# Kernel optimization log

Measured on AMD Instinct MI355X. Metric: run time of the kernel, lower is better.

The kernel has to match this reference:

```python
import jax, jax.numpy as jnp
import numpy as np
import math

D = 1024
B, S = 8, 2048


def setup_inputs() -> dict:
    key = jax.random.key(0)
    ks = jax.random.split(key, 8)
    q = jax.random.normal(ks[0], (B, S, D), dtype=jnp.float32)
    k = jax.random.normal(ks[1], (B, S, D), dtype=jnp.float32)
    v1 = jax.random.normal(ks[2], (B, S, D), dtype=jnp.float32)
    mask = jax.random.normal(ks[3], (1, S, S), dtype=jnp.float32)
    # Linear params: torch Linear stores W as [out, in]; init ~ U(-1/sqrt(in), 1/sqrt(in))
    lim = 1.0 / math.sqrt(D)
    W1 = jax.random.uniform(ks[4], (D, D), jnp.float32, -lim, lim)
    b1 = jax.random.uniform(ks[5], (D,), jnp.float32, -lim, lim)
    W2 = jax.random.uniform(ks[6], (D, D), jnp.float32, -lim, lim)
    b2 = jax.random.uniform(ks[7], (D,), jnp.float32, -lim, lim)
    return {"q": q, "k": k, "v1": v1, "mask": mask,
            "W1": W1, "b1": b1, "W2": W2, "b2": b2}


def _proj(x, W1, b1, W2, b2):
    # linear2(linear1(x)); torch Linear: x @ W.T + b
    h = jnp.einsum('bsd,od->bso', x, W1) + b1
    return jnp.einsum('bsd,od->bso', h, W2) + b2


def reference(q, k, v1, mask, W1, b1, W2, b2):
    qp = _proj(q, W1, b1, W2, b2)          # [B,S,D]
    kp = _proj(k, W1, b1, W2, b2)          # [B,S,D]
    scale = 1.0 / math.sqrt(qp.shape[-1])
    qk = jnp.einsum('bqd,bkd->bqk', qp, kp) * scale  # [B,S,S]
    qk = qk + mask                          # broadcast [1,S,S]
    attn = jax.nn.softmax(qk, axis=-1)
    return jnp.einsum('bqk,bkd->bqd', attn, v1)  # [B,S,D]
```

## Files before the change

kernel.cpp:

```cpp
#include <hip/hip_runtime.h>
#include <hip/hip_bf16.h>

typedef __hip_bfloat16 bf16;
typedef __bf16 bf16x8 __attribute__((ext_vector_type(8)));
typedef float f32x4 __attribute__((ext_vector_type(4)));

constexpr int Bn = 8, Sn = 2048, Dn = 1024;
constexpr int BM = 128, BN = 128, BK = 64;

__global__ void cast_f32_bf16_k(const float* __restrict__ x, bf16* __restrict__ y, int n) {
  int i = (blockIdx.x * blockDim.x + threadIdx.x) * 4;
  if (i >= n) return;
  float4 f = *reinterpret_cast<const float4*>(x + i);
  bf16 tmp[4] = {__float2bfloat16(f.x), __float2bfloat16(f.y),
                 __float2bfloat16(f.z), __float2bfloat16(f.w)};
  *reinterpret_cast<short4*>(y + i) = *reinterpret_cast<const short4*>(tmp);
}

__global__ void transpose_cast_v_k(const float* __restrict__ v, bf16* __restrict__ vt) {
  __shared__ float tile[32][33];
  const int s0 = blockIdx.x * 32, d0 = blockIdx.y * 32, b = blockIdx.z;
  const float* src = v + (size_t)b * Sn * Dn;
  bf16* dst = vt + (size_t)b * Dn * Sn;
  const int tx = threadIdx.x & 31, ty = threadIdx.x >> 5;
  #pragma unroll
  for (int i = 0; i < 4; ++i) {
    int s = ty + i * 8;
    tile[s][tx] = src[(size_t)(s0 + s) * Dn + d0 + tx];
  }
  __syncthreads();
  #pragma unroll
  for (int i = 0; i < 4; ++i) {
    int d = ty + i * 8;
    dst[(size_t)(d0 + d) * Sn + s0 + tx] = __float2bfloat16(tile[tx][d]);
  }
}

#define SBAR()  asm volatile("s_barrier" ::: "memory")
#define LGKM0() asm volatile("s_waitcnt lgkmcnt(0)" ::: "memory")
#define VM0()   asm volatile("s_waitcnt vmcnt(0)" ::: "memory")

#define MFMA16() do {                                                         \
    __builtin_amdgcn_s_setprio(1);                                            \
    _Pragma("unroll")                                                         \
    for (int kk = 0; kk < 2; ++kk)                                            \
      _Pragma("unroll")                                                       \
      for (int mi4 = 0; mi4 < 4; ++mi4)                                       \
        _Pragma("unroll")                                                     \
        for (int n2 = 0; n2 < 2; ++n2)                                        \
          acc[mi4][n2] = __builtin_amdgcn_mfma_f32_16x16x32_bf16(             \
              aF[mi4][kk], bF[n2][kk], acc[mi4][n2], 0, 0, 0);                \
    __builtin_amdgcn_s_setprio(0);                                            \
  } while (0)

#define ITER(cur, T) do {                                                     \
    const bool pf = (T) + 1 < NT;                                             \
    if (pf) {                                                                 \
      stage2((1 - (cur)) * 32768,         Abase, (T) + 1);                    \
      stage2((1 - (cur)) * 32768 + 16384, Bbase, (T) + 1);                    \
    }                                                                         \
    _Pragma("unroll")                                                         \
    for (int mi4 = 0; mi4 < 4; ++mi4) {                                       \
      aF[mi4][0] = *reinterpret_cast<const bf16x8*>(pA0 + (cur)*32768 + mi4*2048); \
      aF[mi4][1] = *reinterpret_cast<const bf16x8*>(pA1 + (cur)*32768 + mi4*2048); \
    }                                                                         \
    _Pragma("unroll")                                                         \
    for (int j = 0; j < 2; ++j) {                                             \
      bF[j][0] = *reinterpret_cast<const bf16x8*>(pB0 + (cur)*32768 + j*2048); \
      bF[j][1] = *reinterpret_cast<const bf16x8*>(pB1 + (cur)*32768 + j*2048); \
    }                                                                         \
    LGKM0();                                                                  \
    MFMA16();                                                                 \
    if (pf) VM0();                                                            \
    SBAR();                                                                   \
  } while (0)

template<int EPI>
__global__ __launch_bounds__(512, 4)
void gemm128_k(const bf16* __restrict__ A, const bf16* __restrict__ BT,
               void* __restrict__ Cv, const float* __restrict__ aux,
               int N, int K, long long sAz, long long sBz, long long sCz,
               float scale, int gx, int gy)
{
  __shared__ __align__(128) bf16 sh[2 * 16384];

  const int nwg = (int)gridDim.x;
  const int flat = (int)blockIdx.x;
  const int swz = (flat & 7) * (nwg >> 3) + (flat >> 3);
  const int tn = swz % gx;
  const int rem = swz / gx;
  const int tm = rem % gy;
  const int z  = rem / gy;

  const int t = threadIdx.x, w = t >> 6, lane = t & 63;
  const int wm = w >> 2, wn = w & 3;
  const int fr = lane & 15, kg = lane >> 4;
  const int m0 = tm * BM, n0 = tn * BN;
  const bf16* Abase = A + (size_t)z * sAz + (size_t)m0 * K;
  const bf16* Bbase = BT + (size_t)z * sBz + (size_t)n0 * K;

  f32x4 acc[4][2];
  const f32x4 fz = {0.f, 0.f, 0.f, 0.f};
  #pragma unroll
  for (int i = 0; i < 4; ++i) { acc[i][0] = fz; acc[i][1] = fz; }
  bf16x8 aF[4][2], bF[2][2];

  const char* shB = (const char*)sh;
  const int swzlo = (fr & 3) << 4;
  const int swzhi = (fr & 4) << 4;
  const int aoff0 = (wm * 64 + fr) * 128 + ((kg * 16) ^ swzlo) + swzhi;
  const int boff0 = 16384 + (wn * 32 + fr) * 128 + ((kg * 16) ^ swzlo) + swzhi;
  const char* pA0 = shB + aoff0;
  const char* pA1 = shB + (aoff0 ^ 64);
  const char* pB0 = shB + boff0;
  const char* pB1 = shB + (boff0 ^ 64);

  int gOff[2];
  #pragma unroll
  for (int i = 0; i < 2; ++i) {
    const int slot = i * 512 + w * 64 + lane;
    const int row = slot >> 3;
    const int cb = (slot & 7) ^ (row & 7);
    gOff[i] = row * K + cb * 8;
  }
  auto stage2 = [&](int dstByte, const bf16* gbase, int kt) {
    const bf16* g0 = gbase + (size_t)kt * BK;
    char* db = (char*)sh + dstByte;
    #pragma unroll
    for (int i = 0; i < 2; ++i) {
      __builtin_amdgcn_global_load_lds(
          (__attribute__((address_space(1))) void*)(g0 + gOff[i]),
          (__attribute__((address_space(3))) void*)(db + (i * 512 + w * 64) * 16),
          16, 0, 0);
    }
  };

  const int NT = K / BK;
  stage2(0,     Abase, 0);
  stage2(16384, Bbase, 0);
  VM0();
  SBAR();

  for (int T = 0; T < NT; T += 2) {
    ITER(0, T);
    ITER(1, T + 1);
  }

  const int or0 = kg * 4;
  if constexpr (EPI == 0) {
    bf16* C = (bf16*)Cv + (size_t)z * sCz;
    #pragma unroll
    for (int mi = 0; mi < 4; ++mi)
      #pragma unroll
      for (int r = 0; r < 4; ++r) {
        const int row = m0 + wm * 64 + mi * 16 + or0 + r;
        #pragma unroll
        for (int nj = 0; nj < 2; ++nj) {
          const int col = n0 + wn * 32 + nj * 16 + fr;
          C[(size_t)row * N + col] = __float2bfloat16(acc[mi][nj][r] + aux[col]);
        }
      }
  } else if constexpr (EPI == 1) {
    bf16* C = (bf16*)Cv + (size_t)z * sCz;
    #pragma unroll
    for (int mi = 0; mi < 4; ++mi)
      #pragma unroll
      for (int r = 0; r < 4; ++r) {
        const int row = m0 + wm * 64 + mi * 16 + or0 + r;
        #pragma unroll
        for (int nj = 0; nj < 2; ++nj) {
          const int col = n0 + wn * 32 + nj * 16 + fr;
          float v = acc[mi][nj][r] * scale + aux[(size_t)row * N + col];
          C[(size_t)row * N + col] = __float2bfloat16(v);
        }
      }
  } else {
    float* C = (float*)Cv + (size_t)z * sCz;
    #pragma unroll
    for (int mi = 0; mi < 4; ++mi)
      #pragma unroll
      for (int r = 0; r < 4; ++r) {
        const int row = m0 + wm * 64 + mi * 16 + or0 + r;
        #pragma unroll
        for (int nj = 0; nj < 2; ++nj) {
          const int col = n0 + wn * 32 + nj * 16 + fr;
          C[(size_t)row * N + col] = acc[mi][nj][r];
        }
      }
  }
}

__global__ __launch_bounds__(256)
void softmax_rows_k(bf16* __restrict__ sc) {
  const size_t row = blockIdx.x;
  bf16* p = sc + row * (size_t)Sn;
  const int t = threadIdx.x;
  unsigned short raw[8];
  *reinterpret_cast<int4*>(raw) = *reinterpret_cast<const int4*>(p + t * 8);
  float x[8];
  float m = -1e30f;
  #pragma unroll
  for (int j = 0; j < 8; ++j) {
    x[j] = __uint_as_float(((unsigned)raw[j]) << 16);
    m = fmaxf(m, x[j]);
  }
  #pragma unroll
  for (int off = 32; off >= 1; off >>= 1) m = fmaxf(m, __shfl_xor(m, off));
  __shared__ float sred[4], ssum[4];
  const int w = t >> 6;
  if ((t & 63) == 0) sred[w] = m;
  __syncthreads();
  m = fmaxf(fmaxf(sred[0], sred[1]), fmaxf(sred[2], sred[3]));
  float e[8], s = 0.f;
  #pragma unroll
  for (int j = 0; j < 8; ++j) { e[j] = __expf(x[j] - m); s += e[j]; }
  #pragma unroll
  for (int off = 32; off >= 1; off >>= 1) s += __shfl_xor(s, off);
  if ((t & 63) == 0) ssum[w] = s;
  __syncthreads();
  s = (ssum[0] + ssum[1]) + (ssum[2] + ssum[3]);
  const float inv = 1.f / s;
  unsigned short o[8];
  #pragma unroll
  for (int j = 0; j < 8; ++j) {
    bf16 hv = __float2bfloat16(e[j] * inv);
    o[j] = *reinterpret_cast<unsigned short*>(&hv);
  }
  *reinterpret_cast<int4*>(p + t * 8) = *reinterpret_cast<const int4*>(o);
}

extern "C" void kernel_launch(void* const* d_in, const int* in_sizes, int n_in,
                              void* d_out, int out_size, void* d_ws, size_t ws_size,
                              hipStream_t stream) {
  const float* q    = (const float*)d_in[0];
  const float* k    = (const float*)d_in[1];
  const float* v1   = (const float*)d_in[2];
  const float* mask = (const float*)d_in[3];
  const float* W1   = (const float*)d_in[4];
  const float* b1   = (const float*)d_in[5];
  const float* W2   = (const float*)d_in[6];
  const float* b2   = (const float*)d_in[7];
  float* out = (float*)d_out;

  const size_t nQKD = (size_t)Bn * Sn * Dn;
  char* ws = (char*)d_ws;
  bf16* qkb = (bf16*)ws;
  bf16* qb  = qkb;
  bf16* kb  = qkb + nQKD;
  bf16* vtb = qkb + 2 * nQKD;
  bf16* hb  = vtb + nQKD;
  bf16* w1b = hb + 2 * nQKD;
  bf16* w2b = w1b + (size_t)Dn * Dn;
  bf16* scb = w2b + (size_t)Dn * Dn;

  dim3 blk(256);
  const int nQK = (int)nQKD;
  cast_f32_bf16_k<<<dim3(nQK / 4 / 256), blk, 0, stream>>>(q, qb, nQK);
  cast_f32_bf16_k<<<dim3(nQK / 4 / 256), blk, 0, stream>>>(k, kb, nQK);
  cast_f32_bf16_k<<<dim3(Dn * Dn / 4 / 256), blk, 0, stream>>>(W1, w1b, Dn * Dn);
  cast_f32_bf16_k<<<dim3(Dn * Dn / 4 / 256), blk, 0, stream>>>(W2, w2b, Dn * Dn);
  transpose_cast_v_k<<<dim3(Sn / 32, Dn / 32, Bn), blk, 0, stream>>>(v1, vtb);

  const int M2 = 2 * Bn * Sn;
  dim3 gblk(512);
  gemm128_k<0><<<dim3((Dn / BN) * (M2 / BM)), gblk, 0, stream>>>(
      qkb, w1b, hb, b1, Dn, Dn, 0, 0, 0, 1.f, Dn / BN, M2 / BM);
  gemm128_k<0><<<dim3((Dn / BN) * (M2 / BM)), gblk, 0, stream>>>(
      hb, w2b, qkb, b2, Dn, Dn, 0, 0, 0, 1.f, Dn / BN, M2 / BM);
  gemm128_k<1><<<dim3(16 * 16 * Bn), gblk, 0, stream>>>(
      qb, kb, scb, mask, Sn, Dn,
      (long long)Sn * Dn, (long long)Sn * Dn, (long long)Sn * Sn, 0.03125f, 16, 16);
  softmax_rows_k<<<dim3(Bn * Sn), blk, 0, stream>>>(scb);
  gemm128_k<2><<<dim3(8 * 16 * Bn), gblk, 0, stream>>>(
      scb, vtb, out, nullptr, Dn, Sn,
      (long long)Sn * Sn, (long long)Dn * Sn, (long long)Sn * Dn, 1.f, 8, 16);
}
```

Before: 402.4 us.

## Fuse softmax into GEMM epilogues and switch to triple-buffered BK=32 pipeline

Result: slower. 427.6 us (+6.3%).

```diff
diff --git a/kernel.cpp b/kernel.cpp
--- a/kernel.cpp
+++ b/kernel.cpp
@@ -6,7 +6,6 @@
 typedef float f32x4 __attribute__((ext_vector_type(4)));
 
 constexpr int Bn = 8, Sn = 2048, Dn = 1024;
-constexpr int BM = 128, BN = 128, BK = 64;
 
 __global__ void cast_f32_bf16_k(const float* __restrict__ x, bf16* __restrict__ y, int n) {
   int i = (blockIdx.x * blockDim.x + threadIdx.x) * 4;
@@ -38,51 +37,17 @@
 
 #define SBAR()  asm volatile("s_barrier" ::: "memory")
 #define LGKM0() asm volatile("s_waitcnt lgkmcnt(0)" ::: "memory")
+#define VM2()   asm volatile("s_waitcnt vmcnt(2)" ::: "memory")
 #define VM0()   asm volatile("s_waitcnt vmcnt(0)" ::: "memory")
 
-#define MFMA16() do {                                                         \
-    __builtin_amdgcn_s_setprio(1);                                            \
-    _Pragma("unroll")                                                         \
-    for (int kk = 0; kk < 2; ++kk)                                            \
-      _Pragma("unroll")                                                       \
-      for (int mi4 = 0; mi4 < 4; ++mi4)                                       \
-        _Pragma("unroll")                                                     \
-        for (int n2 = 0; n2 < 2; ++n2)                                        \
-          acc[mi4][n2] = __builtin_amdgcn_mfma_f32_16x16x32_bf16(             \
-              aF[mi4][kk], bF[n2][kk], acc[mi4][n2], 0, 0, 0);                \
-    __builtin_amdgcn_s_setprio(0);                                            \
-  } while (0)
-
-#define ITER(cur, T) do {                                                     \
-    const bool pf = (T) + 1 < NT;                                             \
-    if (pf) {                                                                 \
-      stage2((1 - (cur)) * 32768,         Abase, (T) + 1);                    \
-      stage2((1 - (cur)) * 32768 + 16384, Bbase, (T) + 1);                    \
-    }                                                                         \
-    _Pragma("unroll")                                                         \
-    for (int mi4 = 0; mi4 < 4; ++mi4) {                                       \
-      aF[mi4][0] = *reinterpret_cast<const bf16x8*>(pA0 + (cur)*32768 + mi4*2048); \
-      aF[mi4][1] = *reinterpret_cast<const bf16x8*>(pA1 + (cur)*32768 + mi4*2048); \
-    }                                                                         \
-    _Pragma("unroll")                                                         \
-    for (int j = 0; j < 2; ++j) {                                             \
-      bF[j][0] = *reinterpret_cast<const bf16x8*>(pB0 + (cur)*32768 + j*2048); \
-      bF[j][1] = *reinterpret_cast<const bf16x8*>(pB1 + (cur)*32768 + j*2048); \
-    }                                                                         \
-    LGKM0();                                                                  \
-    MFMA16();                                                                 \
-    if (pf) VM0();                                                            \
-    SBAR();                                                                   \
-  } while (0)
-
-template<int EPI>
-__global__ __launch_bounds__(512, 4)
+template<int EPI, int K>
+__global__ __launch_bounds__(512, 6)
 void gemm128_k(const bf16* __restrict__ A, const bf16* __restrict__ BT,
                void* __restrict__ Cv, const float* __restrict__ aux,
-               int N, int K, long long sAz, long long sBz, long long sCz,
+               int N, long long sAz, long long sBz, long long sCz,
                float scale, int gx, int gy)
 {
-  __shared__ __align__(128) bf16 sh[2 * 16384];
+  __shared__ __align__(128) bf16 sh[3 * 8192];
 
   const int nwg = (int)gridDim.x;
   const int flat = (int)blockIdx.x;
@@ -95,7 +60,7 @@
   const int t = threadIdx.x, w = t >> 6, lane = t & 63;
   const int wm = w >> 2, wn = w & 3;
   const int fr = lane & 15, kg = lane >> 4;
-  const int m0 = tm * BM, n0 = tn * BN;
+  const int m0 = tm * 128, n0 = tn * 128;
   const bf16* Abase = A + (size_t)z * sAz + (size_t)m0 * K;
   const bf16* Bbase = BT + (size_t)z * sBz + (size_t)n0 * K;
 
@@ -103,47 +68,53 @@
   const f32x4 fz = {0.f, 0.f, 0.f, 0.f};
   #pragma unroll
   for (int i = 0; i < 4; ++i) { acc[i][0] = fz; acc[i][1] = fz; }
-  bf16x8 aF[4][2], bF[2][2];
+  bf16x8 aF[4], bF[2];
 
   const char* shB = (const char*)sh;
-  const int swzlo = (fr & 3) << 4;
-  const int swzhi = (fr & 4) << 4;
-  const int aoff0 = (wm * 64 + fr) * 128 + ((kg * 16) ^ swzlo) + swzhi;
-  const int boff0 = 16384 + (wn * 32 + fr) * 128 + ((kg * 16) ^ swzlo) + swzhi;
-  const char* pA0 = shB + aoff0;
-  const char* pA1 = shB + (aoff0 ^ 64);
-  const char* pB0 = shB + boff0;
-  const char* pB1 = shB + (boff0 ^ 64);
-
-  int gOff[2];
-  #pragma unroll
-  for (int i = 0; i < 2; ++i) {
-    const int slot = i * 512 + w * 64 + lane;
-    const int row = slot >> 3;
-    const int cb = (slot & 7) ^ (row & 7);
-    gOff[i] = row * K + cb * 8;
-  }
-  auto stage2 = [&](int dstByte, const bf16* gbase, int kt) {
-    const bf16* g0 = gbase + (size_t)kt * BK;
-    char* db = (char*)sh + dstByte;
-    #pragma unroll
-    for (int i = 0; i < 2; ++i) {
-      __builtin_amdgcn_global_load_lds(
-          (__attribute__((address_space(1))) void*)(g0 + gOff[i]),
-          (__attribute__((address_space(3))) void*)(db + (i * 512 + w * 64) * 16),
-          16, 0, 0);
+  const char* pA = shB + (wm * 64 + fr) * 64 + kg * 16;
+  const char* pB = shB + 8192 + (wn * 32 + fr) * 64 + kg * 16;
+
+  const int gOff = (t >> 2) * K + (t & 3) * 8;
+  const int dOff = t * 16;
+  auto stage = [&](int dstByte, const bf16* gbase, int kt) {
+    const bf16* g0 = gbase + kt * 32;
+    __builtin_amdgcn_global_load_lds(
+        (__attribute__((address_space(1))) void*)(g0 + gOff),
+        (__attribute__((address_space(3))) void*)((char*)sh + dstByte + dOff),
+        16, 0, 0);
+  };
+
+  constexpr int NT = K / 32;
+  stage(0,     Abase, 0); stage(8192,         Bbase, 0);
+  stage(16384, Abase, 1); stage(16384 + 8192, Bbase, 1);
+  VM2();
+  SBAR();
+
+  #pragma unroll
+  for (int T = 0; T < NT; ++T) {
+    const int bb = (T % 3) * 16384;
+    if (T + 2 < NT) {
+      const int pb = ((T + 2) % 3) * 16384;
+      stage(pb,        Abase, T + 2);
+      stage(pb + 8192, Bbase, T + 2);
     }
-  };
-
-  const int NT = K / BK;
-  stage2(0,     Abase, 0);
-  stage2(16384, Bbase, 0);
-  VM0();
-  SBAR();
-
-  for (int T = 0; T < NT; T += 2) {
-    ITER(0, T);
-    ITER(1, T + 1);
+    #pragma unroll
+    for (int mi4 = 0; mi4 < 4; ++mi4)
+      aF[mi4] = *reinterpret_cast<const bf16x8*>(pA + bb + mi4 * 1024);
+    #pragma unroll
+    for (int nj = 0; nj < 2; ++nj)
+      bF[nj] = *reinterpret_cast<const bf16x8*>(pB + bb + nj * 1024);
+    LGKM0();
+    __builtin_amdgcn_s_setprio(1);
+    #pragma unroll
+    for (int mi4 = 0; mi4 < 4; ++mi4)
+      #pragma unroll
+      for (int nj = 0; nj < 2; ++nj)
+        acc[mi4][nj] = __builtin_amdgcn_mfma_f32_16x16x32_bf16(
+            aF[mi4], bF[nj], acc[mi4][nj], 0, 0, 0);
+    __builtin_amdgcn_s_setprio(0);
+    if (T + 2 < NT) { VM2(); } else if (T + 1 < NT) { VM0(); }
+    SBAR();
   }
 
   const int or0 = kg * 4;
@@ -170,63 +141,44 @@
         #pragma unroll
         for (int nj = 0; nj < 2; ++nj) {
           const int col = n0 + wn * 32 + nj * 16 + fr;
-          float v = acc[mi][nj][r] * scale + aux[(size_t)row * N + col];
+          float v = __expf(acc[mi][nj][r] * scale + aux[(size_t)row * N + col]);
           C[(size_t)row * N + col] = __float2bfloat16(v);
         }
       }
   } else {
     float* C = (float*)Cv + (size_t)z * sCz;
+    const float* Zb = aux + (size_t)z * Sn;
     #pragma unroll
     for (int mi = 0; mi < 4; ++mi)
       #pragma unroll
       for (int r = 0; r < 4; ++r) {
         const int row = m0 + wm * 64 + mi * 16 + or0 + r;
+        const float invZ = 1.0f / Zb[row];
         #pragma unroll
         for (int nj = 0; nj < 2; ++nj) {
           const int col = n0 + wn * 32 + nj * 16 + fr;
-          C[(size_t)row * N + col] = acc[mi][nj][r];
+          C[(size_t)row * N + col] = acc[mi][nj][r] * invZ;
         }
       }
   }
 }
 
 __global__ __launch_bounds__(256)
-void softmax_rows_k(bf16* __restrict__ sc) {
+void rowsum_k(const bf16* __restrict__ sc, float* __restrict__ Z) {
   const size_t row = blockIdx.x;
-  bf16* p = sc + row * (size_t)Sn;
+  const bf16* p = sc + row * (size_t)Sn;
   const int t = threadIdx.x;
   unsigned short raw[8];
   *reinterpret_cast<int4*>(raw) = *reinterpret_cast<const int4*>(p + t * 8);
-  float x[8];
-  float m = -1e30f;
-  #pragma unroll
-  for (int j = 0; j < 8; ++j) {
-    x[j] = __uint_as_float(((unsigned)raw[j]) << 16);
-    m = fmaxf(m, x[j]);
-  }
-  #pragma unroll
-  for (int off = 32; off >= 1; off >>= 1) m = fmaxf(m, __shfl_xor(m, off));
-  __shared__ float sred[4], ssum[4];
-  const int w = t >> 6;
-  if ((t & 63) == 0) sred[w] = m;
+  float s = 0.f;
+  #pragma unroll
+  for (int j = 0; j < 8; ++j) s += __uint_as_float(((unsigned)raw[j]) << 16);
+  #pragma unroll
+  for (int off = 32; off >= 1; off >>= 1) s += __shfl_xor(s, off);
+  __shared__ float ssum[4];
+  if ((t & 63) == 0) ssum[t >> 6] = s;
   __syncthreads();
-  m = fmaxf(fmaxf(sred[0], sred[1]), fmaxf(sred[2], sred[3]));
-  float e[8], s = 0.f;
-  #pragma unroll
-  for (int j = 0; j < 8; ++j) { e[j] = __expf(x[j] - m); s += e[j]; }
-  #pragma unroll
-  for (int off = 32; off >= 1; off >>= 1) s += __shfl_xor(s, off);
-  if ((t & 63) == 0) ssum[w] = s;
-  __syncthreads();
-  s = (ssum[0] + ssum[1]) + (ssum[2] + ssum[3]);
-  const float inv = 1.f / s;
-  unsigned short o[8];
-  #pragma unroll
-  for (int j = 0; j < 8; ++j) {
-    bf16 hv = __float2bfloat16(e[j] * inv);
-    o[j] = *reinterpret_cast<unsigned short*>(&hv);
-  }
-  *reinterpret_cast<int4*>(p + t * 8) = *reinterpret_cast<const int4*>(o);
+  if (t == 0) Z[row] = (ssum[0] + ssum[1]) + (ssum[2] + ssum[3]);
 }
 
 extern "C" void kernel_launch(void* const* d_in, const int* in_sizes, int n_in,
@@ -252,6 +204,7 @@
   bf16* w1b = hb + 2 * nQKD;
   bf16* w2b = w1b + (size_t)Dn * Dn;
   bf16* scb = w2b + (size_t)Dn * Dn;
+  float* Zb = (float*)(scb + (size_t)Bn * Sn * Sn);
 
   dim3 blk(256);
   const int nQK = (int)nQKD;
@@ -263,15 +216,15 @@
 
   const int M2 = 2 * Bn * Sn;
   dim3 gblk(512);
-  gemm128_k<0><<<dim3((Dn / BN) * (M2 / BM)), gblk, 0, stream>>>(
-      qkb, w1b, hb, b1, Dn, Dn, 0, 0, 0, 1.f, Dn / BN, M2 / BM);
-  gemm128_k<0><<<dim3((Dn / BN) * (M2 / BM)), gblk, 0, stream>>>(
-      hb, w2b, qkb, b2, Dn, Dn, 0, 0, 0, 1.f, Dn / BN, M2 / BM);
-  gemm128_k<1><<<dim3(16 * 16 * Bn), gblk, 0, stream>>>(
-      qb, kb, scb, mask, Sn, Dn,
+  gemm128_k<0, Dn><<<dim3((Dn / 128) * (M2 / 128)), gblk, 0, stream>>>(
+      qkb, w1b, hb, b1, Dn, 0, 0, 0, 1.f, Dn / 128, M2 / 128);
+  gemm128_k<0, Dn><<<dim3((Dn / 128) * (M2 / 128)), gblk, 0, stream>>>(
+      hb, w2b, qkb, b2, Dn, 0, 0, 0, 1.f, Dn / 128, M2 / 128);
+  gemm128_k<1, Dn><<<dim3(16 * 16 * Bn), gblk, 0, stream>>>(
+      qb, kb, scb, mask, Sn,
       (long long)Sn * Dn, (long long)Sn * Dn, (long long)Sn * Sn, 0.03125f, 16, 16);
-  softmax_rows_k<<<dim3(Bn * Sn), blk, 0, stream>>>(scb);
-  gemm128_k<2><<<dim3(8 * 16 * Bn), gblk, 0, stream>>>(
-      scb, vtb, out, nullptr, Dn, Sn,
+  rowsum_k<<<dim3(Bn * Sn), blk, 0, stream>>>(scb, Zb);
+  gemm128_k<2, Sn><<<dim3(8 * 16 * Bn), gblk, 0, stream>>>(
+      scb, vtb, out, Zb, Dn,
       (long long)Sn * Sn, (long long)Dn * Sn, (long long)Sn * Dn, 1.f, 8, 16);
 }
```

## Compose the two linear layers into one weight and defer softmax normalization

Applied to the files above, without the earlier changes.

New measurement: 341.3 us. -15.2%, faster.

```diff
diff --git a/kernel.cpp b/kernel.cpp
--- a/kernel.cpp
+++ b/kernel.cpp
@@ -7,6 +7,16 @@
 
 constexpr int Bn = 8, Sn = 2048, Dn = 1024;
 constexpr int BM = 128, BN = 128, BK = 64;
+
+__global__ void cast2_f32_bf16_k(const float* __restrict__ x0, const float* __restrict__ x1,
+                                 bf16* __restrict__ y, int n ) {
+  int i = (blockIdx.x * blockDim.x + threadIdx.x) * 4;
+  const float* src = (i < n) ? (x0 + i) : (x1 + (i - n));
+  float4 f = *reinterpret_cast<const float4*>(src);
+  bf16 tmp[4] = {__float2bfloat16(f.x), __float2bfloat16(f.y),
+                 __float2bfloat16(f.z), __float2bfloat16(f.w)};
+  *reinterpret_cast<short4*>(y + i) = *reinterpret_cast<const short4*>(tmp);
+}
 
 __global__ void cast_f32_bf16_k(const float* __restrict__ x, bf16* __restrict__ y, int n) {
   int i = (blockIdx.x * blockDim.x + threadIdx.x) * 4;
@@ -17,23 +27,40 @@
   *reinterpret_cast<short4*>(y + i) = *reinterpret_cast<const short4*>(tmp);
 }
 
-__global__ void transpose_cast_v_k(const float* __restrict__ v, bf16* __restrict__ vt) {
+__global__ void transpose_cast_k(const float* __restrict__ src0, bf16* __restrict__ dst0,
+                                 int R, int C) {
   __shared__ float tile[32][33];
-  const int s0 = blockIdx.x * 32, d0 = blockIdx.y * 32, b = blockIdx.z;
-  const float* src = v + (size_t)b * Sn * Dn;
-  bf16* dst = vt + (size_t)b * Dn * Sn;
+  const int r0 = blockIdx.x * 32, c0 = blockIdx.y * 32, b = blockIdx.z;
+  const float* src = src0 + (size_t)b * R * C;
+  bf16* dst = dst0 + (size_t)b * C * R;
   const int tx = threadIdx.x & 31, ty = threadIdx.x >> 5;
   #pragma unroll
   for (int i = 0; i < 4; ++i) {
-    int s = ty + i * 8;
-    tile[s][tx] = src[(size_t)(s0 + s) * Dn + d0 + tx];
+    int r = ty + i * 8;
+    tile[r][tx] = src[(size_t)(r0 + r) * C + c0 + tx];
   }
   __syncthreads();
   #pragma unroll
   for (int i = 0; i < 4; ++i) {
-    int d = ty + i * 8;
-    dst[(size_t)(d0 + d) * Sn + s0 + tx] = __float2bfloat16(tile[tx][d]);
-  }
+    int c = ty + i * 8;
+    dst[(size_t)(c0 + c) * R + r0 + tx] = __float2bfloat16(tile[tx][c]);
+  }
+}
+
+__global__ __launch_bounds__(256)
+void bias_compose_k(const float* __restrict__ W2, const float* __restrict__ b1,
+                    const float* __restrict__ b2, float* __restrict__ bc) {
+  const int row = blockIdx.x;
+  const int t = threadIdx.x;
+  float4 wv = *reinterpret_cast<const float4*>(W2 + (size_t)row * Dn + t * 4);
+  float4 bv = *reinterpret_cast<const float4*>(b1 + t * 4);
+  float s = wv.x * bv.x + wv.y * bv.y + wv.z * bv.z + wv.w * bv.w;
+  #pragma unroll
+  for (int off = 32; off >= 1; off >>= 1) s += __shfl_xor(s, off);
+  __shared__ float ssum[4];
+  if ((t & 63) == 0) ssum[t >> 6] = s;
+  __syncthreads();
+  if (t == 0) bc[row] = (ssum[0] + ssum[1]) + (ssum[2] + ssum[3]) + b2[row];
 }
 
 #define SBAR()  asm volatile("s_barrier" ::: "memory")
@@ -170,63 +197,57 @@
         #pragma unroll
         for (int nj = 0; nj < 2; ++nj) {
           const int col = n0 + wn * 32 + nj * 16 + fr;
-          float v = acc[mi][nj][r] * scale + aux[(size_t)row * N + col];
+          float v = __expf(acc[mi][nj][r] * scale + aux[(size_t)row * N + col]);
           C[(size_t)row * N + col] = __float2bfloat16(v);
         }
       }
+  } else if constexpr (EPI == 2) {
+    float* C = (float*)Cv + (size_t)z * sCz;
+    const float* Zb = aux + (size_t)z * Sn;
+    #pragma unroll
+    for (int mi = 0; mi < 4; ++mi)
+      #pragma unroll
+      for (int r = 0; r < 4; ++r) {
+        const int row = m0 + wm * 64 + mi * 16 + or0 + r;
+        const float invZ = 1.0f / Zb[row];
+        #pragma unroll
+        for (int nj = 0; nj < 2; ++nj) {
+          const int col = n0 + wn * 32 + nj * 16 + fr;
+          C[(size_t)row * N + col] = acc[mi][nj][r] * invZ;
+        }
+      }
   } else {
-    float* C = (float*)Cv + (size_t)z * sCz;
-    #pragma unroll
-    for (int mi = 0; mi < 4; ++mi)
-      #pragma unroll
-      for (int r = 0; r < 4; ++r) {
-        const int row = m0 + wm * 64 + mi * 16 + or0 + r;
-        #pragma unroll
-        for (int nj = 0; nj < 2; ++nj) {
-          const int col = n0 + wn * 32 + nj * 16 + fr;
-          C[(size_t)row * N + col] = acc[mi][nj][r];
+    bf16* C = (bf16*)Cv + (size_t)z * sCz;
+    #pragma unroll
+    for (int mi = 0; mi < 4; ++mi)
+      #pragma unroll
+      for (int r = 0; r < 4; ++r) {
+        const int row = m0 + wm * 64 + mi * 16 + or0 + r;
+        #pragma unroll
+        for (int nj = 0; nj < 2; ++nj) {
+          const int col = n0 + wn * 32 + nj * 16 + fr;
+          C[(size_t)row * N + col] = __float2bfloat16(acc[mi][nj][r]);
         }
       }
   }
 }
 
 __global__ __launch_bounds__(256)
-void softmax_rows_k(bf16* __restrict__ sc) {
+void rowsum_k(const bf16* __restrict__ sc, float* __restrict__ Z) {
   const size_t row = blockIdx.x;
-  bf16* p = sc + row * (size_t)Sn;
+  const bf16* p = sc + row * (size_t)Sn;
   const int t = threadIdx.x;
   unsigned short raw[8];
   *reinterpret_cast<int4*>(raw) = *reinterpret_cast<const int4*>(p + t * 8);
-  float x[8];
-  float m = -1e30f;
-  #pragma unroll
-  for (int j = 0; j < 8; ++j) {
-    x[j] = __uint_as_float(((unsigned)raw[j]) << 16);
-    m = fmaxf(m, x[j]);
-  }
-  #pragma unroll
-  for (int off = 32; off >= 1; off >>= 1) m = fmaxf(m, __shfl_xor(m, off));
-  __shared__ float sred[4], ssum[4];
-  const int w = t >> 6;
-  if ((t & 63) == 0) sred[w] = m;
+  float s = 0.f;
+  #pragma unroll
+  for (int j = 0; j < 8; ++j) s += __uint_as_float(((unsigned)raw[j]) << 16);
+  #pragma unroll
+  for (int off = 32; off >= 1; off >>= 1) s += __shfl_xor(s, off);
+  __shared__ float ssum[4];
+  if ((t & 63) == 0) ssum[t >> 6] = s;
   __syncthreads();
-  m = fmaxf(fmaxf(sred[0], sred[1]), fmaxf(sred[2], sred[3]));
-  float e[8], s = 0.f;
-  #pragma unroll
-  for (int j = 0; j < 8; ++j) { e[j] = __expf(x[j] - m); s += e[j]; }
-  #pragma unroll
-  for (int off = 32; off >= 1; off >>= 1) s += __shfl_xor(s, off);
-  if ((t & 63) == 0) ssum[w] = s;
-  __syncthreads();
-  s = (ssum[0] + ssum[1]) + (ssum[2] + ssum[3]);
-  const float inv = 1.f / s;
-  unsigned short o[8];
-  #pragma unroll
-  for (int j = 0; j < 8; ++j) {
-    bf16 hv = __float2bfloat16(e[j] * inv);
-    o[j] = *reinterpret_cast<unsigned short*>(&hv);
-  }
-  *reinterpret_cast<int4*>(p + t * 8) = *reinterpret_cast<const int4*>(o);
+  if (t == 0) Z[row] = (ssum[0] + ssum[1]) + (ssum[2] + ssum[3]);
 }
 
 extern "C" void kernel_launch(void* const* d_in, const int* in_sizes, int n_in,
@@ -244,34 +265,35 @@
 
   const size_t nQKD = (size_t)Bn * Sn * Dn;
   char* ws = (char*)d_ws;
-  bf16* qkb = (bf16*)ws;
-  bf16* qb  = qkb;
-  bf16* kb  = qkb + nQKD;
-  bf16* vtb = qkb + 2 * nQKD;
-  bf16* hb  = vtb + nQKD;
-  bf16* w1b = hb + 2 * nQKD;
-  bf16* w2b = w1b + (size_t)Dn * Dn;
-  bf16* scb = w2b + (size_t)Dn * Dn;
+  bf16* qkb  = (bf16*)ws;
+  bf16* vtb  = qkb + 2 * nQKD;
+  bf16* hb   = vtb + nQKD;
+  bf16* w1t  = hb + 2 * nQKD;
+  bf16* w2b  = w1t + (size_t)Dn * Dn;
+  bf16* wcb  = w2b + (size_t)Dn * Dn;
+  bf16* scb  = wcb + (size_t)Dn * Dn;
+  float* Zb  = (float*)(scb + (size_t)Bn * Sn * Sn);
+  float* bcb = Zb + (size_t)Bn * Sn;
 
   dim3 blk(256);
   const int nQK = (int)nQKD;
-  cast_f32_bf16_k<<<dim3(nQK / 4 / 256), blk, 0, stream>>>(q, qb, nQK);
-  cast_f32_bf16_k<<<dim3(nQK / 4 / 256), blk, 0, stream>>>(k, kb, nQK);
-  cast_f32_bf16_k<<<dim3(Dn * Dn / 4 / 256), blk, 0, stream>>>(W1, w1b, Dn * Dn);
+  cast2_f32_bf16_k<<<dim3(2 * nQK / 4 / 256), blk, 0, stream>>>(q, k, qkb, nQK);
   cast_f32_bf16_k<<<dim3(Dn * Dn / 4 / 256), blk, 0, stream>>>(W2, w2b, Dn * Dn);
-  transpose_cast_v_k<<<dim3(Sn / 32, Dn / 32, Bn), blk, 0, stream>>>(v1, vtb);
+  transpose_cast_k<<<dim3(Dn / 32, Dn / 32, 1), blk, 0, stream>>>(W1, w1t, Dn, Dn);
+  transpose_cast_k<<<dim3(Sn / 32, Dn / 32, Bn), blk, 0, stream>>>(v1, vtb, Sn, Dn);
+  bias_compose_k<<<dim3(Dn), blk, 0, stream>>>(W2, b1, b2, bcb);
 
   const int M2 = 2 * Bn * Sn;
   dim3 gblk(512);
-  gemm128_k<0><<<dim3((Dn / BN) * (M2 / BM)), gblk, 0, stream>>>(
-      qkb, w1b, hb, b1, Dn, Dn, 0, 0, 0, 1.f, Dn / BN, M2 / BM);
-  gemm128_k<0><<<dim3((Dn / BN) * (M2 / BM)), gblk, 0, stream>>>(
-      hb, w2b, qkb, b2, Dn, Dn, 0, 0, 0, 1.f, Dn / BN, M2 / BM);
+  gemm128_k<3><<<dim3(8 * 8), gblk, 0, stream>>>(
+      w2b, w1t, wcb, nullptr, Dn, Dn, 0, 0, 0, 1.f, 8, 8);
+  gemm128_k<0><<<dim3(8 * (M2 / 128)), gblk, 0, stream>>>(
+      qkb, wcb, hb, bcb, Dn, Dn, 0, 0, 0, 1.f, 8, M2 / 128);
   gemm128_k<1><<<dim3(16 * 16 * Bn), gblk, 0, stream>>>(
-      qb, kb, scb, mask, Sn, Dn,
+      hb, hb + nQKD, scb, mask, Sn, Dn,
       (long long)Sn * Dn, (long long)Sn * Dn, (long long)Sn * Sn, 0.03125f, 16, 16);
-  softmax_rows_k<<<dim3(Bn * Sn), blk, 0, stream>>>(scb);
+  rowsum_k<<<dim3(Bn * Sn), blk, 0, stream>>>(scb, Zb);
   gemm128_k<2><<<dim3(8 * 16 * Bn), gblk, 0, stream>>>(
-      scb, vtb, out, nullptr, Dn, Sn,
+      scb, vtb, out, Zb, Dn, Sn,
       (long long)Sn * Sn, (long long)Dn * Sn, (long long)Sn * Dn, 1.f, 8, 16);
 }
```
